# Optimization experiments

Measured on AMD Instinct MI355X. Metric: run time of the kernel, lower is better.

Reference implementation:

```python
import jax, jax.numpy as jnp
import numpy as np

THRESH = 0.2  # contact probability threshold from _make_graph default


def setup_inputs() -> dict:
    key = jax.random.key(0)
    ks = jax.random.split(key, 10)
    L, D, K, M = 1024, 640, 32, 64
    S = jax.random.normal(ks[0], (L, D), jnp.float32)
    P = jax.random.uniform(ks[1], (L, L), jnp.float32)
    P = 0.5 * (P + P.T)  # symmetric base-pair probability matrix
    xyz = jax.random.normal(ks[2], (L, 3), jnp.float32) * 10.0  # Angstrom-scale C1' coords
    rbf_mu = jnp.linspace(0.0, 30.0, K).astype(jnp.float32)     # RBF centers over 0-30 A
    rbf_sigma = jax.random.uniform(ks[3], (K,), jnp.float32, 0.5, 2.0)
    W_edge = jax.random.normal(ks[4], (K + 2, M), jnp.float32) * 0.05
    b_edge = jnp.zeros((M,), jnp.float32)
    W_node = jax.random.normal(ks[5], (D, M), jnp.float32) * 0.05
    w_out = jax.random.normal(ks[6], (M,), jnp.float32) * 0.1
    return {"S": S, "P": P, "xyz": xyz, "rbf_mu": rbf_mu, "rbf_sigma": rbf_sigma,
            "W_edge": W_edge, "b_edge": b_edge, "W_node": W_node, "w_out": w_out}


def reference(S, P, xyz, rbf_mu, rbf_sigma, W_edge, b_edge, W_node, w_out):
    """Graph construction (_make_graph) + one SE3-style gated coordinate update.

    Edges: backbone (j == i+1, etype=0, pij=1) and high-prob contacts
    (P[i,j] > THRESH, j > i+2, etype=1, pij=P[i,j]). Edge scalars are
    [etype, pij, rbf(d)] exactly as in _make_graph; edge vectors are
    xyz[j]-xyz[i]. Computed in dense masked form for jit-compatibility.
    """
    L = xyz.shape[0]
    rel = xyz[None, :, :] - xyz[:, None, :]                      # (L,L,3) xyz[j]-xyz[i]
    # safe norm: eps avoids nan grad on zero diagonal (diagonal is masked out anyway)
    d = jnp.sqrt(jnp.sum(rel * rel, axis=-1, keepdims=True) + 1e-12)  # (L,L,1)
    rbf_feat = jnp.exp(-(d - rbf_mu) ** 2 / (2.0 * rbf_sigma ** 2))   # (L,L,K)

    idx = jnp.arange(L)
    backbone = idx[None, :] == idx[:, None] + 1                  # j == i+1
    contact = (P > THRESH) & (idx[None, :] > idx[:, None] + 2)   # skip j <= i+2
    mask = backbone | contact                                    # (L,L)

    etype = contact.astype(S.dtype)                              # 0 backbone, 1 contact
    pij = jnp.where(backbone, jnp.asarray(1.0, S.dtype), P)
    e_scalar = jnp.concatenate([etype[..., None], pij[..., None], rbf_feat], axis=-1)  # (L,L,K+2)

    # gather-compute: message from edge scalars + destination-node scalars
    node_proj = S @ W_node                                       # (L,M)
    msg = jax.nn.relu(jnp.einsum('ijk,km->ijm', e_scalar, W_edge) + b_edge
                      + node_proj[None, :, :])                   # (L,L,M)
    gate = jax.nn.sigmoid(msg @ w_out) * mask.astype(S.dtype)    # (L,L)

    # scatter: equivariant coordinate update, sum of gated edge vectors per node
    xyz_out = xyz + jnp.einsum('ij,ijc->ic', gate, rel)          # (L,3)
    return xyz_out
```

## Files before the change

kernel.cpp:

```cpp
#include <hip/hip_runtime.h>
#include <math.h>

#define LL 1024
#define DD 640
#define KK 32
#define MM 64
#define THRESH 0.2f

#define NPROJ_OFF  0
#define NPROJC_OFF (NPROJ_OFF + LL * MM)
#define WRT_OFF    (NPROJC_OFF + LL * MM)
#define W1_OFF     (WRT_OFF + 1024)
#define MU_OFF     (W1_OFF + MM)
#define NIS2_OFF   (MU_OFF + KK)
#define XYZ4_OFF   (NIS2_OFF + KK)

typedef float f32x4_t __attribute__((ext_vector_type(4)));
typedef short bf16x8_t __attribute__((ext_vector_type(8)));

union FragU { unsigned int u[4]; bf16x8_t v; };

#if __has_builtin(__builtin_amdgcn_sqrtf)
#define FSQRT __builtin_amdgcn_sqrtf
#else
#define FSQRT sqrtf
#endif

__device__ __forceinline__ unsigned int pack_bf(float hi, float lo) {
    return __builtin_amdgcn_perm(__float_as_uint(hi), __float_as_uint(lo), 0x07060302u);
}

__global__ __launch_bounds__(256) void prep_gemm(
    const float* __restrict__ S, const float* __restrict__ xyz,
    const float* __restrict__ rbf_mu, const float* __restrict__ rbf_sigma,
    const float* __restrict__ W_edge, const float* __restrict__ b_edge,
    const float* __restrict__ W_node, float* __restrict__ ws)
{
    const int b = blockIdx.x;
    const int t = threadIdx.x;
    if (b < 64) {
        const int lane = t & 63;
        const int wave = t >> 6;
        const int id   = b * 4 + wave;
        const int r0   = (id >> 2) * 16;
        const int n0   = (id & 3) * 16;
        const int col  = lane & 15;
        const int quad = lane >> 4;

        f32x4_t acc = {0.f, 0.f, 0.f, 0.f};
        const float* arow = S + (size_t)(r0 + col) * DD + quad * 8;
        const float* bcol = W_node + (size_t)(quad * 8) * MM + n0 + col;

        #pragma unroll 2
        for (int ks = 0; ks < 20; ++ks) {
            const float4 a0 = *(const float4*)(arow + ks * 32);
            const float4 a1 = *(const float4*)(arow + ks * 32 + 4);
            FragU A;
            A.u[0] = pack_bf(a0.y, a0.x); A.u[1] = pack_bf(a0.w, a0.z);
            A.u[2] = pack_bf(a1.y, a1.x); A.u[3] = pack_bf(a1.w, a1.z);
            const float* bk = bcol + (size_t)ks * 32 * MM;
            const float b0 = bk[0 * MM], b1 = bk[1 * MM], b2 = bk[2 * MM], b3 = bk[3 * MM];
            const float b4 = bk[4 * MM], b5 = bk[5 * MM], b6 = bk[6 * MM], b7 = bk[7 * MM];
            FragU B;
            B.u[0] = pack_bf(b1, b0); B.u[1] = pack_bf(b3, b2);
            B.u[2] = pack_bf(b5, b4); B.u[3] = pack_bf(b7, b6);
            acc = __builtin_amdgcn_mfma_f32_16x16x32_bf16(A.v, B.v, acc, 0, 0, 0);
        }
        const float bias = b_edge[n0 + col];
        const float w0   = W_edge[n0 + col];
        #pragma unroll
        for (int r = 0; r < 4; ++r) {
            const int row = r0 + quad * 4 + r;
            const float v = acc[r] + bias;
            ws[NPROJ_OFF  + (size_t)row * MM + n0 + col] = v;
            ws[NPROJC_OFF + (size_t)row * MM + n0 + col] = v + w0;
        }
    } else {
        unsigned short* wrt = (unsigned short*)(ws + WRT_OFF);
        if (t < MM) ws[W1_OFF + t] = W_edge[MM + t];
        if (t < KK) {
            ws[MU_OFF + t] = rbf_mu[t];
            const float s = rbf_sigma[t];
            ws[NIS2_OFF + t] = -1.0f / (2.0f * s * s);
        }
        for (int idx = t; idx < KK * MM; idx += 256) {
            const int m = idx >> 5, k = idx & 31;
            unsigned int u = __float_as_uint(W_edge[(2 + k) * MM + m]);
            u = (u + 0x7fffu + ((u >> 16) & 1u)) >> 16;
            wrt[idx] = (unsigned short)u;
        }
        for (int n = t; n < LL; n += 256) {
            float4 v;
            v.x = xyz[3 * n + 0]; v.y = xyz[3 * n + 1];
            v.z = xyz[3 * n + 2]; v.w = 0.0f;
            *(float4*)(ws + XYZ4_OFF + 4 * n) = v;
        }
    }
}

__global__ __launch_bounds__(256, 3) void edge_kernel(
    const float* __restrict__ P, const float* __restrict__ w_out,
    const float* __restrict__ ws, float* __restrict__ out)
{
    const int tid  = threadIdx.x;
    const int lane = tid & 63;
    const int wave = tid >> 6;
    const int quad = lane >> 4;
    const int col  = lane & 15;
    __shared__ float sred[4][3];

    const float* __restrict__ nproj  = ws + NPROJ_OFF;
    const float* __restrict__ nprojc = ws + NPROJC_OFF;
    const float4* __restrict__ xyz4  = (const float4*)(ws + XYZ4_OFF);
    const unsigned short* __restrict__ wrt = (const unsigned short*)(ws + WRT_OFF);

    FragU ar[4];
    float w1r[16], wvr[16];
    float muj[8], nis2[8];
    #pragma unroll
    for (int mt = 0; mt < 4; ++mt) {
        const uint4 w = *(const uint4*)(wrt + (mt * 16 + col) * KK + quad * 8);
        ar[mt].u[0] = w.x; ar[mt].u[1] = w.y; ar[mt].u[2] = w.z; ar[mt].u[3] = w.w;
        const f32x4_t w1 = *(const f32x4_t*)(ws + W1_OFF + mt * 16 + quad * 4);
        const f32x4_t wo = *(const f32x4_t*)(w_out + mt * 16 + quad * 4);
        #pragma unroll
        for (int r = 0; r < 4; ++r) { w1r[mt * 4 + r] = w1[r]; wvr[mt * 4 + r] = wo[r]; }
    }
    #pragma unroll
    for (int j = 0; j < 8; ++j) {
        muj[j]  = ws[MU_OFF + quad * 8 + j];
        nis2[j] = ws[NIS2_OFF + quad * 8 + j];
    }
    #pragma unroll
    for (int mt = 0; mt < 4; ++mt) {
        asm volatile("" : "+v"(ar[mt].u[0]), "+v"(ar[mt].u[1]),
                          "+v"(ar[mt].u[2]), "+v"(ar[mt].u[3]));
        asm volatile("" : "+v"(w1r[mt*4+0]), "+v"(w1r[mt*4+1]),
                          "+v"(w1r[mt*4+2]), "+v"(w1r[mt*4+3]));
        asm volatile("" : "+v"(wvr[mt*4+0]), "+v"(wvr[mt*4+1]),
                          "+v"(wvr[mt*4+2]), "+v"(wvr[mt*4+3]));
    }
    #pragma unroll
    for (int j = 0; j < 8; j += 4) {
        asm volatile("" : "+v"(muj[j]), "+v"(muj[j+1]), "+v"(muj[j+2]), "+v"(muj[j+3]));
        asm volatile("" : "+v"(nis2[j]), "+v"(nis2[j+1]), "+v"(nis2[j+2]), "+v"(nis2[j+3]));
    }

    const int i = (int)blockIdx.x;
    const float4 xo = xyz4[i];
    const float xi0 = xo.x, xi1 = xo.y, xi2 = xo.z;
    float ax = 0.f, ay = 0.f, az = 0.f;
    const int len = (LL - 1) - i;

    for (int base = wave * 64; base < len; base += 256) {
        const int jo = base + lane;
        const bool valid = jo < len;
        const int jc = valid ? (i + 1 + jo) : (LL - 1);
        const float p_own = P[(size_t)i * LL + jc];
        const float4 xj = xyz4[jc];
        const float rx = xj.x - xi0, ry = xj.y - xi1, rz = xj.z - xi2;
        const bool msk = valid && ((jo == 0) || ((jo >= 2) && (p_own > THRESH)));

        float res[4];
        #pragma unroll
        for (int ct = 0; ct < 4; ++ct) {
            const int jo_n = base + ct * 16 + col;
            int jc_n = i + 1 + jo_n;
            jc_n = (jc_n < LL) ? jc_n : (LL - 1);
            const float p_n = P[(size_t)i * LL + jc_n];
            const float4 xn = xyz4[jc_n];
            const float dx = xn.x - xi0, dy = xn.y - xi1, dz = xn.z - xi2;
            const float d_n = FSQRT(fmaf(dx, dx, fmaf(dy, dy, fmaf(dz, dz, 1e-12f))));
            const bool bb = (jo_n == 0);
            const float peff = bb ? 1.0f : p_n;
            const float* bp = bb ? nproj : nprojc;

            float r[8];
            #pragma unroll
            for (int j = 0; j < 8; ++j) {
                const float t0 = d_n - muj[j];
                r[j] = __expf(t0 * t0 * nis2[j]);
            }
            FragU bf;
            bf.u[0] = pack_bf(r[1], r[0]); bf.u[1] = pack_bf(r[3], r[2]);
            bf.u[2] = pack_bf(r[5], r[4]); bf.u[3] = pack_bf(r[7], r[6]);

            const float* npr = bp + (size_t)jc_n * MM;
            float g = 0.0f;
            #pragma unroll
            for (int mt = 0; mt < 4; ++mt) {
                f32x4_t c0 = *(const f32x4_t*)(npr + mt * 16 + quad * 4);
                c0[0] = fmaf(peff, w1r[mt*4+0], c0[0]);
                c0[1] = fmaf(peff, w1r[mt*4+1], c0[1]);
                c0[2] = fmaf(peff, w1r[mt*4+2], c0[2]);
                c0[3] = fmaf(peff, w1r[mt*4+3], c0[3]);
                c0 = __builtin_amdgcn_mfma_f32_16x16x32_bf16(ar[mt].v, bf.v, c0, 0, 0, 0);
                g = fmaf(fmaxf(c0[0], 0.f), wvr[mt*4+0], g);
                g = fmaf(fmaxf(c0[1], 0.f), wvr[mt*4+1], g);
                g = fmaf(fmaxf(c0[2], 0.f), wvr[mt*4+2], g);
                g = fmaf(fmaxf(c0[3], 0.f), wvr[mt*4+3], g);
            }
            g += __shfl_xor(g, 16, 64);
            g += __shfl_xor(g, 32, 64);
            res[ct] = g;
        }
        float gd = res[0];
        gd = (quad == 1) ? res[1] : gd;
        gd = (quad == 2) ? res[2] : gd;
        gd = (quad == 3) ? res[3] : gd;
        const float gate = msk ? (1.0f / (1.0f + __expf(-gd))) : 0.0f;
        ax = fmaf(gate, rx, ax);
        ay = fmaf(gate, ry, ay);
        az = fmaf(gate, rz, az);
    }

    #pragma unroll
    for (int off = 32; off > 0; off >>= 1) {
        ax += __shfl_down(ax, off, 64);
        ay += __shfl_down(ay, off, 64);
        az += __shfl_down(az, off, 64);
    }
    if (lane == 0) { sred[wave][0] = ax; sred[wave][1] = ay; sred[wave][2] = az; }
    __syncthreads();
    if (tid == 0) {
        const float tx = (sred[0][0] + sred[1][0]) + (sred[2][0] + sred[3][0]);
        const float ty = (sred[0][1] + sred[1][1]) + (sred[2][1] + sred[3][1]);
        const float tz = (sred[0][2] + sred[1][2]) + (sred[2][2] + sred[3][2]);
        out[i * 3 + 0] = xi0 + tx;
        out[i * 3 + 1] = xi1 + ty;
        out[i * 3 + 2] = xi2 + tz;
    }
}

extern "C" void kernel_launch(void* const* d_in, const int* in_sizes, int n_in,
                              void* d_out, int out_size, void* d_ws, size_t ws_size,
                              hipStream_t stream) {
    const float* S         = (const float*)d_in[0];
    const float* P         = (const float*)d_in[1];
    const float* xyz       = (const float*)d_in[2];
    const float* rbf_mu    = (const float*)d_in[3];
    const float* rbf_sigma = (const float*)d_in[4];
    const float* W_edge    = (const float*)d_in[5];
    const float* b_edge    = (const float*)d_in[6];
    const float* W_node    = (const float*)d_in[7];
    const float* w_out     = (const float*)d_in[8];
    float* out = (float*)d_out;
    float* ws  = (float*)d_ws;

    prep_gemm<<<65, 256, 0, stream>>>(S, xyz, rbf_mu, rbf_sigma,
                                      W_edge, b_edge, W_node, ws);
    edge_kernel<<<LL, 256, 0, stream>>>(P, w_out, ws, out);
}
```

Baseline: 99.86 us.

## Split each row across two blocks with atomic output and expanded-quadratic exp2 RBF

Each source row is now processed by two blocks (2*L grid), each striding by 512 columns. Per-block partial sums are accumulated into an output pre-initialised with xyz via atomicAdd. The RBF exponent is rewritten as a quadratic in d with precomputed log2e-scaled coefficients so it can use exp2 directly. P loads are reduced to one per lane per tile and prefetched one iteration ahead, and occupancy is raised to 4 blocks per SM. Aims to improve load balance on the triangular workload and cut ALU work. In exchange it adds atomics, and the expanded quadratic can lose precision through cancellation.

```diff
diff --git a/kernel.cpp b/kernel.cpp
--- a/kernel.cpp
+++ b/kernel.cpp
@@ -6,14 +6,16 @@
 #define KK 32
 #define MM 64
 #define THRESH 0.2f
+#define LOG2E 1.4426950408889634f
 
 #define NPROJ_OFF  0
 #define NPROJC_OFF (NPROJ_OFF + LL * MM)
 #define WRT_OFF    (NPROJC_OFF + LL * MM)
 #define W1_OFF     (WRT_OFF + 1024)
-#define MU_OFF     (W1_OFF + MM)
-#define NIS2_OFF   (MU_OFF + KK)
-#define XYZ4_OFF   (NIS2_OFF + KK)
+#define EA_OFF     (W1_OFF + MM)
+#define EB_OFF     (EA_OFF + KK)
+#define EC_OFF     (EB_OFF + KK)
+#define XYZ4_OFF   (EC_OFF + KK)
 
 typedef float f32x4_t __attribute__((ext_vector_type(4)));
 typedef short bf16x8_t __attribute__((ext_vector_type(8)));
@@ -26,6 +28,12 @@
 #define FSQRT sqrtf
 #endif
 
+#if __has_builtin(__builtin_amdgcn_exp2f)
+#define EXP2F __builtin_amdgcn_exp2f
+#else
+#define EXP2F(x) __expf((x) * 0.6931471805599453f)
+#endif
+
 __device__ __forceinline__ unsigned int pack_bf(float hi, float lo) {
     return __builtin_amdgcn_perm(__float_as_uint(hi), __float_as_uint(lo), 0x07060302u);
 }
@@ -34,7 +42,8 @@
     const float* __restrict__ S, const float* __restrict__ xyz,
     const float* __restrict__ rbf_mu, const float* __restrict__ rbf_sigma,
     const float* __restrict__ W_edge, const float* __restrict__ b_edge,
-    const float* __restrict__ W_node, float* __restrict__ ws)
+    const float* __restrict__ W_node, float* __restrict__ ws,
+    float* __restrict__ out)
 {
     const int b = blockIdx.x;
     const int t = threadIdx.x;
@@ -79,9 +88,12 @@
         unsigned short* wrt = (unsigned short*)(ws + WRT_OFF);
         if (t < MM) ws[W1_OFF + t] = W_edge[MM + t];
         if (t < KK) {
-            ws[MU_OFF + t] = rbf_mu[t];
-            const float s = rbf_sigma[t];
-            ws[NIS2_OFF + t] = -1.0f / (2.0f * s * s);
+            const float s  = rbf_sigma[t];
+            const float m_ = rbf_mu[t];
+            const float inv = 1.0f / (2.0f * s * s);
+            ws[EA_OFF + t] = -LOG2E * inv;
+            ws[EB_OFF + t] =  2.0f * LOG2E * inv * m_;
+            ws[EC_OFF + t] = -LOG2E * inv * m_ * m_;
         }
         for (int idx = t; idx < KK * MM; idx += 256) {
             const int m = idx >> 5, k = idx & 31;
@@ -95,10 +107,11 @@
             v.z = xyz[3 * n + 2]; v.w = 0.0f;
             *(float4*)(ws + XYZ4_OFF + 4 * n) = v;
         }
-    }
-}
-
-__global__ __launch_bounds__(256, 3) void edge_kernel(
+        for (int idx = t; idx < 3 * LL; idx += 256) out[idx] = xyz[idx];
+    }
+}
+
+__global__ __launch_bounds__(256, 4) void edge_kernel2(
     const float* __restrict__ P, const float* __restrict__ w_out,
     const float* __restrict__ ws, float* __restrict__ out)
 {
@@ -116,7 +129,7 @@
 
     FragU ar[4];
     float w1r[16], wvr[16];
-    float muj[8], nis2[8];
+    float aj[8], bj[8], cj[8];
     #pragma unroll
     for (int mt = 0; mt < 4; ++mt) {
         const uint4 w = *(const uint4*)(wrt + (mt * 16 + col) * KK + quad * 8);
@@ -128,8 +141,9 @@
     }
     #pragma unroll
     for (int j = 0; j < 8; ++j) {
-        muj[j]  = ws[MU_OFF + quad * 8 + j];
-        nis2[j] = ws[NIS2_OFF + quad * 8 + j];
+        aj[j] = ws[EA_OFF + quad * 8 + j];
+        bj[j] = ws[EB_OFF + quad * 8 + j];
+        cj[j] = ws[EC_OFF + quad * 8 + j];
     }
     #pragma unroll
     for (int mt = 0; mt < 4; ++mt) {
@@ -142,23 +156,50 @@
     }
     #pragma unroll
     for (int j = 0; j < 8; j += 4) {
-        asm volatile("" : "+v"(muj[j]), "+v"(muj[j+1]), "+v"(muj[j+2]), "+v"(muj[j+3]));
-        asm volatile("" : "+v"(nis2[j]), "+v"(nis2[j+1]), "+v"(nis2[j+2]), "+v"(nis2[j+3]));
-    }
-
-    const int i = (int)blockIdx.x;
+        asm volatile("" : "+v"(aj[j]), "+v"(aj[j+1]), "+v"(aj[j+2]), "+v"(aj[j+3]));
+        asm volatile("" : "+v"(bj[j]), "+v"(bj[j+1]), "+v"(bj[j+2]), "+v"(bj[j+3]));
+        asm volatile("" : "+v"(cj[j]), "+v"(cj[j+1]), "+v"(cj[j+2]), "+v"(cj[j+3]));
+    }
+
+    const int g = (int)blockIdx.x;
+    const int i = g >> 1;
+    const int h = g & 1;
     const float4 xo = xyz4[i];
     const float xi0 = xo.x, xi1 = xo.y, xi2 = xo.z;
+    const int len = (LL - 1) - i;
     float ax = 0.f, ay = 0.f, az = 0.f;
-    const int len = (LL - 1) - i;
-
-    for (int base = wave * 64; base < len; base += 256) {
+    const float* __restrict__ prow = P + (size_t)i * LL;
+
+    const int b0 = (h * 4 + wave) * 64;
+
+    float pp[4];
+    #pragma unroll
+    for (int ct = 0; ct < 4; ++ct) {
+        int jc = i + 1 + b0 + ct * 16 + col;
+        jc = (jc < LL) ? jc : (LL - 1);
+        pp[ct] = prow[jc];
+    }
+
+    for (int base = b0; base < len; base += 512) {
+        float pc[4];
+        #pragma unroll
+        for (int ct = 0; ct < 4; ++ct) pc[ct] = pp[ct];
+        #pragma unroll
+        for (int ct = 0; ct < 4; ++ct) {
+            int jc = i + 1 + base + 512 + ct * 16 + col;
+            jc = (jc < LL) ? jc : (LL - 1);
+            pp[ct] = prow[jc];
+        }
+
         const int jo = base + lane;
         const bool valid = jo < len;
-        const int jc = valid ? (i + 1 + jo) : (LL - 1);
-        const float p_own = P[(size_t)i * LL + jc];
-        const float4 xj = xyz4[jc];
+        const int jc_o = valid ? (i + 1 + jo) : (LL - 1);
+        const float4 xj = xyz4[jc_o];
         const float rx = xj.x - xi0, ry = xj.y - xi1, rz = xj.z - xi2;
+        float p_own = pc[0];
+        p_own = (quad == 1) ? pc[1] : p_own;
+        p_own = (quad == 2) ? pc[2] : p_own;
+        p_own = (quad == 3) ? pc[3] : p_own;
         const bool msk = valid && ((jo == 0) || ((jo >= 2) && (p_own > THRESH)));
 
         float res[4];
@@ -167,26 +208,23 @@
             const int jo_n = base + ct * 16 + col;
             int jc_n = i + 1 + jo_n;
             jc_n = (jc_n < LL) ? jc_n : (LL - 1);
-            const float p_n = P[(size_t)i * LL + jc_n];
             const float4 xn = xyz4[jc_n];
             const float dx = xn.x - xi0, dy = xn.y - xi1, dz = xn.z - xi2;
             const float d_n = FSQRT(fmaf(dx, dx, fmaf(dy, dy, fmaf(dz, dz, 1e-12f))));
+            const float d2 = d_n * d_n;
             const bool bb = (jo_n == 0);
-            const float peff = bb ? 1.0f : p_n;
-            const float* bp = bb ? nproj : nprojc;
-
-            float r[8];
+            const float peff = bb ? 1.0f : pc[ct];
+            const float* npr = (bb ? nproj : nprojc) + (size_t)jc_n * MM;
+
+            float e[8];
             #pragma unroll
-            for (int j = 0; j < 8; ++j) {
-                const float t0 = d_n - muj[j];
-                r[j] = __expf(t0 * t0 * nis2[j]);
-            }
+            for (int j = 0; j < 8; ++j)
+                e[j] = EXP2F(fmaf(aj[j], d2, fmaf(bj[j], d_n, cj[j])));
             FragU bf;
-            bf.u[0] = pack_bf(r[1], r[0]); bf.u[1] = pack_bf(r[3], r[2]);
-            bf.u[2] = pack_bf(r[5], r[4]); bf.u[3] = pack_bf(r[7], r[6]);
-
-            const float* npr = bp + (size_t)jc_n * MM;
-            float g = 0.0f;
+            bf.u[0] = pack_bf(e[1], e[0]); bf.u[1] = pack_bf(e[3], e[2]);
+            bf.u[2] = pack_bf(e[5], e[4]); bf.u[3] = pack_bf(e[7], e[6]);
+
+            float gg = 0.0f;
             #pragma unroll
             for (int mt = 0; mt < 4; ++mt) {
                 f32x4_t c0 = *(const f32x4_t*)(npr + mt * 16 + quad * 4);
@@ -195,14 +233,14 @@
                 c0[2] = fmaf(peff, w1r[mt*4+2], c0[2]);
                 c0[3] = fmaf(peff, w1r[mt*4+3], c0[3]);
                 c0 = __builtin_amdgcn_mfma_f32_16x16x32_bf16(ar[mt].v, bf.v, c0, 0, 0, 0);
-                g = fmaf(fmaxf(c0[0], 0.f), wvr[mt*4+0], g);
-                g = fmaf(fmaxf(c0[1], 0.f), wvr[mt*4+1], g);
-                g = fmaf(fmaxf(c0[2], 0.f), wvr[mt*4+2], g);
-                g = fmaf(fmaxf(c0[3], 0.f), wvr[mt*4+3], g);
+                gg = fmaf(fmaxf(c0[0], 0.f), wvr[mt*4+0], gg);
+                gg = fmaf(fmaxf(c0[1], 0.f), wvr[mt*4+1], gg);
+                gg = fmaf(fmaxf(c0[2], 0.f), wvr[mt*4+2], gg);
+                gg = fmaf(fmaxf(c0[3], 0.f), wvr[mt*4+3], gg);
             }
-            g += __shfl_xor(g, 16, 64);
-            g += __shfl_xor(g, 32, 64);
-            res[ct] = g;
+            gg += __shfl_xor(gg, 16, 64);
+            gg += __shfl_xor(gg, 32, 64);
+            res[ct] = gg;
         }
         float gd = res[0];
         gd = (quad == 1) ? res[1] : gd;
@@ -226,9 +264,9 @@
         const float tx = (sred[0][0] + sred[1][0]) + (sred[2][0] + sred[3][0]);
         const float ty = (sred[0][1] + sred[1][1]) + (sred[2][1] + sred[3][1]);
         const float tz = (sred[0][2] + sred[1][2]) + (sred[2][2] + sred[3][2]);
-        out[i * 3 + 0] = xi0 + tx;
-        out[i * 3 + 1] = xi1 + ty;
-        out[i * 3 + 2] = xi2 + tz;
+        atomicAdd(out + i * 3 + 0, tx);
+        atomicAdd(out + i * 3 + 1, ty);
+        atomicAdd(out + i * 3 + 2, tz);
     }
 }
 
@@ -248,6 +286,6 @@
     float* ws  = (float*)d_ws;
 
     prep_gemm<<<65, 256, 0, stream>>>(S, xyz, rbf_mu, rbf_sigma,
-                                      W_edge, b_edge, W_node, ws);
-    edge_kernel<<<LL, 256, 0, stream>>>(P, w_out, ws, out);
-}
+                                      W_edge, b_edge, W_node, ws, out);
+    edge_kernel2<<<2 * LL, 256, 0, stream>>>(P, w_out, ws, out);
+}
```

Measured after the change: 105.6 us. +5.7%, slower.
